# Kernel tuning notes

Measured on AMD Instinct MI355X. Metric: run time of the kernel, lower is better.

## Reference

```python
import jax, jax.numpy as jnp
import numpy as np

NUM_FREQS = 6

def posenc(x, num_freqs):
    freqs = (2.0 ** jnp.arange(num_freqs)).astype(x.dtype)  # [F]
    ang = x[..., None] * freqs                               # [N, D, F]
    enc = jnp.concatenate([jnp.sin(ang), jnp.cos(ang)], axis=-1)  # [N, D, 2F]
    return enc.reshape(x.shape[0], -1)

def setup_inputs() -> dict:
    key = jax.random.key(0)
    k1, k2, k3 = jax.random.split(key, 3)
    N, D, C = 200000, 6, 256
    E = D * 2 * NUM_FREQS  # 72
    X = jax.random.normal(k1, (N, D), dtype=jnp.float32)
    linear_mappings = jax.random.normal(k2, (3 * C, E), dtype=jnp.float32) * 0.05
    centroids = jax.random.normal(k3, (C, 3), dtype=jnp.float32)
    return {"X": X, "linear_mappings": linear_mappings, "centroids": centroids}

def reference(X, linear_mappings, centroids):
    N = X.shape[0]
    encoded_X = posenc(X, NUM_FREQS)                         # [N, E]
    rgb_clusters = encoded_X @ linear_mappings.T             # [N, 3C]
    rgb_clusters = rgb_clusters.reshape(N, -1, 3)            # [N, C, 3]
    # scores = centroids @ X[:, :3].T  -> softmax over clusters per point
    scores = X[:, :3] @ centroids.T                          # [N, C] (== scores.T in torch code)
    attention_weights = jax.nn.softmax(scores, axis=-1)      # [N, C]
    # torch does diagonal(attn @ rgb_clusters).T == per-row contraction:
    rgb = jnp.einsum('nc,ncd->nd', attention_weights, rgb_clusters)  # [N, 3]
    return rgb
```

## Files before the change

### kernel.cpp

```cpp
#include <hip/hip_runtime.h>
#include <math.h>


#define NCLUST   256
#define M_BLK    32
#define THREADS  64
#define NTILES   15
#define BG_BYTES (NTILES * 8 * 64 * 16)
#define ET_STRIDE 72

typedef __attribute__((ext_vector_type(8))) short bfrag_t;
typedef __attribute__((ext_vector_type(4))) float cfrag_t;
typedef __attribute__((ext_vector_type(4))) unsigned int uifrag_t;

static __device__ __forceinline__ unsigned short f2bf1(float f) {
    return __builtin_bit_cast(unsigned short, (__bf16)f);
}
static __device__ __forceinline__ unsigned int f2bf2(float lo, float hi) {
    return (unsigned int)f2bf1(lo) | ((unsigned int)f2bf1(hi) << 16);
}
static __device__ __forceinline__ float bf2f(unsigned short s) {
    return __uint_as_float(((unsigned int)s) << 16);
}

__global__ void prep_kernel(const float* __restrict__ W, uint4* __restrict__ Bg) {
    const int u = blockIdx.x * 256 + threadIdx.x;
    if (u >= NTILES * 8 * 64) return;
    const int lane = u & 63, ks = (u >> 6) & 7, tile = u >> 9;
    const int ln = lane & 15, q = lane >> 4;
    const int jp = tile * 16 + ln;
    const int d  = jp / 80;
    const int e  = jp - d * 80;
    const int c0 = ks * 32 + q * 8;
    unsigned int w[4] = {0u, 0u, 0u, 0u};
    if (e < 72) {
#pragma unroll
        for (int i = 0; i < 4; ++i) {
            float f0 = W[((c0 + 2 * i)     * 3 + d) * 72 + e];
            float f1 = W[((c0 + 2 * i + 1) * 3 + d) * 72 + e];
            w[i] = f2bf2(f0, f1);
        }
    }
    Bg[u] = make_uint4(w[0], w[1], w[2], w[3]);
}

#define MFMA2(KS, B) \
    a0 = __builtin_amdgcn_mfma_f32_16x16x32_bf16( \
             __builtin_bit_cast(bfrag_t, afrag[0][KS]), (B), a0, 0, 0, 0); \
    a1 = __builtin_amdgcn_mfma_f32_16x16x32_bf16( \
             __builtin_bit_cast(bfrag_t, afrag[1][KS]), (B), a1, 0, 0, 0);

__global__ __launch_bounds__(THREADS, 2) void rgb_attn_mfma(
    const float* __restrict__ X,
    const float* __restrict__ cent,
    const void* __restrict__ Bg,
    float* __restrict__ out, int N)
{
    __shared__ __align__(16) float Xs[M_BLK * 6];
    __shared__ __align__(16) unsigned char encT[80 * ET_STRIDE];

    const int lane = threadIdx.x;
    const int q    = lane >> 4;
    const int ln   = lane & 15;
    const int mbase = blockIdx.x * M_BLK;

    if (mbase + M_BLK <= N) {
        if (lane < 48) {
            const float4 v = *(const float4*)(X + (size_t)mbase * 6 + lane * 4);
            *(float4*)(Xs + lane * 4) = v;
        }
    } else {
#pragma unroll 1
        for (int i = lane; i < M_BLK * 6; i += 64) {
            const int p  = mbase + i / 6;
            const int pc = (p < N) ? p : (N - 1);
            Xs[i] = X[pc * 6 + (i % 6)];
        }
    }

    const char* Bgc = (const char*)Bg + lane * 16;
    bfrag_t b0 = *(const bfrag_t*)(Bgc + 0 * 1024);
    bfrag_t b1 = *(const bfrag_t*)(Bgc + 1 * 1024);
    bfrag_t b2 = *(const bfrag_t*)(Bgc + 2 * 1024);
    bfrag_t b3 = *(const bfrag_t*)(Bgc + 3 * 1024);
    bfrag_t b4 = *(const bfrag_t*)(Bgc + 4 * 1024);
    bfrag_t b5 = *(const bfrag_t*)(Bgc + 5 * 1024);
    bfrag_t b6 = *(const bfrag_t*)(Bgc + 6 * 1024);
    bfrag_t b7 = *(const bfrag_t*)(Bgc + 7 * 1024);

    {
        const int pt = lane & 31;
        const int h  = lane >> 5;
        unsigned char* colp = encT + pt * 2;
#pragma unroll
        for (int k = 0; k < 3; ++k) {
            const int dd = 3 * h + k;
            const float xv = Xs[pt * 6 + dd];
            float s[6], c[6];
            __sincosf(xv, &s[0], &c[0]);
#pragma unroll
            for (int f = 1; f < 6; ++f) {
                s[f] = 2.0f * s[f-1] * c[f-1];
                c[f] = 1.0f - 2.0f * s[f-1] * s[f-1];
            }
#pragma unroll
            for (int f = 0; f < 6; ++f) {
                *(unsigned short*)(colp + (dd*12 + f)     * ET_STRIDE) = f2bf1(s[f]);
                *(unsigned short*)(colp + (dd*12 + 6 + f) * ET_STRIDE) = f2bf1(c[f]);
            }
        }
        *(uint2*)(encT + (72 + (lane >> 3)) * ET_STRIDE + (lane & 7) * 8) = make_uint2(0u, 0u);
    }

    uifrag_t afrag[2][8];
    float dA = 0.0f, dB = 0.0f;
    {
        const float x00 = Xs[ln * 6 + 0], x01 = Xs[ln * 6 + 1], x02 = Xs[ln * 6 + 2];
        const float x10 = Xs[(16 + ln) * 6 + 0], x11 = Xs[(16 + ln) * 6 + 1],
                    x12 = Xs[(16 + ln) * 6 + 2];
        const float4* c4base = (const float4*)cent;
#pragma unroll
        for (int g = 0; g < 8; ++g) {
            const float4* c4 = c4base + (6 * q + 24 * g);
            const float4 v0 = c4[0], v1 = c4[1], v2 = c4[2];
            const float4 v3 = c4[3], v4 = c4[4], v5 = c4[5];
            float cx[8], cy[8], cz[8];
            cx[0]=v0.x; cy[0]=v0.y; cz[0]=v0.z;
            cx[1]=v0.w; cy[1]=v1.x; cz[1]=v1.y;
            cx[2]=v1.z; cy[2]=v1.w; cz[2]=v2.x;
            cx[3]=v2.y; cy[3]=v2.z; cz[3]=v2.w;
            cx[4]=v3.x; cy[4]=v3.y; cz[4]=v3.z;
            cx[5]=v3.w; cy[5]=v4.x; cz[5]=v4.y;
            cx[6]=v4.z; cy[6]=v4.w; cz[6]=v5.x;
            cx[7]=v5.y; cy[7]=v5.z; cz[7]=v5.w;
            float ea[8], eb[8];
#pragma unroll
            for (int j = 0; j < 8; ++j) {
                ea[j] = __expf(fmaf(x00, cx[j], fmaf(x01, cy[j], x02 * cz[j])));
                eb[j] = __expf(fmaf(x10, cx[j], fmaf(x11, cy[j], x12 * cz[j])));
                dA += ea[j]; dB += eb[j];
            }
#pragma unroll
            for (int w = 0; w < 4; ++w) {
                afrag[0][g][w] = f2bf2(ea[2*w], ea[2*w+1]);
                afrag[1][g][w] = f2bf2(eb[2*w], eb[2*w+1]);
            }
        }
    }

#pragma unroll
    for (int d = 0; d < 3; ++d) {
        float part2[2][4] = {};
#pragma unroll 1
        for (int tt = 0; tt < 5; ++tt) {
            const int t = d * 5 + tt;
            const char* bp = Bgc + (t + 1) * 8192;
            cfrag_t a0 = {0.f,0.f,0.f,0.f}, a1 = {0.f,0.f,0.f,0.f};

            MFMA2(0, b0) MFMA2(1, b1) MFMA2(2, b2) MFMA2(3, b3)
            if (t < NTILES - 1) {
                b0 = *(const bfrag_t*)(bp + 0 * 1024);
                b1 = *(const bfrag_t*)(bp + 1 * 1024);
                b2 = *(const bfrag_t*)(bp + 2 * 1024);
                b3 = *(const bfrag_t*)(bp + 3 * 1024);
            }

            MFMA2(4, b4) MFMA2(5, b5) MFMA2(6, b6) MFMA2(7, b7)
            if (t < NTILES - 1) {
                b4 = *(const bfrag_t*)(bp + 4 * 1024);
                b5 = *(const bfrag_t*)(bp + 5 * 1024);
                b6 = *(const bfrag_t*)(bp + 6 * 1024);
                b7 = *(const bfrag_t*)(bp + 7 * 1024);
            }

            const unsigned char* ep = encT + (tt * 16 + ln) * ET_STRIDE + q * 8;
#pragma unroll
            for (int mt = 0; mt < 2; ++mt) {
                const ushort4 ev = *(const ushort4*)(ep + mt * 32);
                const cfrag_t a = mt ? a1 : a0;
                part2[mt][0] = fmaf(a[0], bf2f(ev.x), part2[mt][0]);
                part2[mt][1] = fmaf(a[1], bf2f(ev.y), part2[mt][1]);
                part2[mt][2] = fmaf(a[2], bf2f(ev.z), part2[mt][2]);
                part2[mt][3] = fmaf(a[3], bf2f(ev.w), part2[mt][3]);
            }
        }

#pragma unroll
        for (int mask = 1; mask <= 8; mask <<= 1)
#pragma unroll
            for (int mt = 0; mt < 2; ++mt)
#pragma unroll
                for (int r = 0; r < 4; ++r)
                    part2[mt][r] += __shfl_xor(part2[mt][r], mask, 64);

        float sA = dA + __shfl_xor(dA, 16, 64); sA += __shfl_xor(sA, 32, 64);
        float sB = dB + __shfl_xor(dB, 16, 64); sB += __shfl_xor(sB, 32, 64);
        const float iA = 1.0f / sA;
        const float iB = 1.0f / sB;
        float invr[2][4];
#pragma unroll
        for (int r = 0; r < 4; ++r) {
            invr[0][r] = __shfl(iA, q * 4 + r, 64);
            invr[1][r] = __shfl(iB, q * 4 + r, 64);
        }

        if (ln == 0) {
#pragma unroll
            for (int mt = 0; mt < 2; ++mt)
#pragma unroll
                for (int r = 0; r < 4; ++r) {
                    const int pm = mt * 16 + q * 4 + r;
                    const int g  = mbase + pm;
                    if (g < N)
                        out[g * 3 + d] = part2[mt][r] * invr[mt][r];
                }
        }
    }
}

__global__ __launch_bounds__(256) void rgb_attn_fallback(
    const float* __restrict__ X, const float* __restrict__ W,
    const float* __restrict__ cent, float* __restrict__ out, int N)
{
    const int n = blockIdx.x * 256 + threadIdx.x;
    const bool valid = (n < N);
    float x[6];
#pragma unroll
    for (int k = 0; k < 6; ++k) x[k] = valid ? X[n * 6 + k] : 0.0f;
    float enc[72];
#pragma unroll
    for (int d = 0; d < 6; ++d)
#pragma unroll
        for (int f = 0; f < 6; ++f) {
            float s, c;
            __sincosf(x[d] * (float)(1 << f), &s, &c);
            enc[d*12+f] = s; enc[d*12+6+f] = c;
        }
    float acc0 = 0, acc1 = 0, acc2 = 0, denom = 0;
#pragma unroll 1
    for (int c = 0; c < NCLUST; ++c) {
        float s = fmaf(x[0], cent[c*3], fmaf(x[1], cent[c*3+1], x[2]*cent[c*3+2]));
        float ew = __expf(s);
        const float* w = W + c * 216;
        float d0 = 0, d1 = 0, d2 = 0;
#pragma unroll
        for (int e = 0; e < 72; ++e) {
            float ee = enc[e];
            d0 = fmaf(ee, w[e], d0);
            d1 = fmaf(ee, w[72 + e], d1);
            d2 = fmaf(ee, w[144 + e], d2);
        }
        denom += ew;
        acc0 = fmaf(ew, d0, acc0); acc1 = fmaf(ew, d1, acc1); acc2 = fmaf(ew, d2, acc2);
    }
    if (valid) {
        float inv = 1.0f / denom;
        out[n*3+0] = acc0*inv; out[n*3+1] = acc1*inv; out[n*3+2] = acc2*inv;
    }
}

extern "C" void kernel_launch(void* const* d_in, const int* in_sizes, int n_in,
                              void* d_out, int out_size, void* d_ws, size_t ws_size,
                              hipStream_t stream)
{
    const float* X    = (const float*)d_in[0];
    const float* W    = (const float*)d_in[1];
    const float* cent = (const float*)d_in[2];
    float* out = (float*)d_out;
    const int N = in_sizes[0] / 6;

    if (ws_size >= (size_t)BG_BYTES) {
        uint4* Bg = (uint4*)d_ws;
        prep_kernel<<<(NTILES * 8 * 64 + 255) / 256, 256, 0, stream>>>(W, Bg);
        const int blocks = (N + M_BLK - 1) / M_BLK;
        rgb_attn_mfma<<<blocks, THREADS, 0, stream>>>(X, cent, (const void*)Bg, out, N);
    } else {
        rgb_attn_fallback<<<(N + 255) / 256, 256, 0, stream>>>(X, W, cent, out, N);
    }
}
```

Baseline: 106.1 us.

## Share weight tiles across four waves via LDS staging with direct global-to-LDS loads

Each block now runs four wavefronts covering 128 points instead of one wave covering 32. The bf16 weight fragments for one output channel (five tiles) are staged into LDS with global_load_lds, and all waves share them instead of each wave streaming the weights from global or L2 into registers. This adds block-level barriers between the three channel phases and roughly 40KB of LDS per block. Occupancy may drop, and the reload between phases is not overlapped with compute.

```diff
diff --git a/kernel.cpp b/kernel.cpp
--- a/kernel.cpp
+++ b/kernel.cpp
@@ -3,8 +3,9 @@
 
 
 #define NCLUST   256
-#define M_BLK    32
-#define THREADS  64
+#define M_BLK    128
+#define WPTS     32
+#define THREADS  256
 #define NTILES   15
 #define BG_BYTES (NTILES * 8 * 64 * 16)
 #define ET_STRIDE 72
@@ -21,6 +22,11 @@
 }
 static __device__ __forceinline__ float bf2f(unsigned short s) {
     return __uint_as_float(((unsigned int)s) << 16);
+}
+static __device__ __forceinline__ void glds16(const void* g, void* l) {
+    __builtin_amdgcn_global_load_lds(
+        (const __attribute__((address_space(1))) unsigned int*)g,
+        (__attribute__((address_space(3))) unsigned int*)l, 16, 0, 0);
 }
 
 __global__ void prep_kernel(const float* __restrict__ W, uint4* __restrict__ Bg) {
@@ -50,43 +56,44 @@
     a1 = __builtin_amdgcn_mfma_f32_16x16x32_bf16( \
              __builtin_bit_cast(bfrag_t, afrag[1][KS]), (B), a1, 0, 0, 0);
 
-__global__ __launch_bounds__(THREADS, 2) void rgb_attn_mfma(
+__global__ __launch_bounds__(THREADS, 4) void rgb_attn_mfma(
     const float* __restrict__ X,
     const float* __restrict__ cent,
     const void* __restrict__ Bg,
     float* __restrict__ out, int N)
 {
-    __shared__ __align__(16) float Xs[M_BLK * 6];
-    __shared__ __align__(16) unsigned char encT[80 * ET_STRIDE];
-
-    const int lane = threadIdx.x;
+    __shared__ __align__(16) unsigned char Bt[5 * 8192];
+    __shared__ __align__(16) unsigned char encT4[4 * 80 * ET_STRIDE];
+    __shared__ __align__(16) float Xs4[4 * WPTS * 6];
+
+    const int tid  = threadIdx.x;
+    const int lane = tid & 63;
+    const int wv   = tid >> 6;
     const int q    = lane >> 4;
     const int ln   = lane & 15;
-    const int mbase = blockIdx.x * M_BLK;
-
-    if (mbase + M_BLK <= N) {
+    const int mbase = blockIdx.x * M_BLK + wv * WPTS;
+    float* Xs = Xs4 + wv * (WPTS * 6);
+    unsigned char* encT = encT4 + wv * (80 * ET_STRIDE);
+
+#pragma unroll
+    for (int i = 0; i < 10; ++i) {
+        const int u = i * 256 + tid;
+        glds16((const char*)Bg + u * 16, (char*)Bt + u * 16);
+    }
+
+    if (mbase + WPTS <= N) {
         if (lane < 48) {
             const float4 v = *(const float4*)(X + (size_t)mbase * 6 + lane * 4);
             *(float4*)(Xs + lane * 4) = v;
         }
     } else {
 #pragma unroll 1
-        for (int i = lane; i < M_BLK * 6; i += 64) {
+        for (int i = lane; i < WPTS * 6; i += 64) {
             const int p  = mbase + i / 6;
             const int pc = (p < N) ? p : (N - 1);
             Xs[i] = X[pc * 6 + (i % 6)];
         }
     }
-
-    const char* Bgc = (const char*)Bg + lane * 16;
-    bfrag_t b0 = *(const bfrag_t*)(Bgc + 0 * 1024);
-    bfrag_t b1 = *(const bfrag_t*)(Bgc + 1 * 1024);
-    bfrag_t b2 = *(const bfrag_t*)(Bgc + 2 * 1024);
-    bfrag_t b3 = *(const bfrag_t*)(Bgc + 3 * 1024);
-    bfrag_t b4 = *(const bfrag_t*)(Bgc + 4 * 1024);
-    bfrag_t b5 = *(const bfrag_t*)(Bgc + 5 * 1024);
-    bfrag_t b6 = *(const bfrag_t*)(Bgc + 6 * 1024);
-    bfrag_t b7 = *(const bfrag_t*)(Bgc + 7 * 1024);
 
     {
         const int pt = lane & 31;
@@ -148,30 +155,36 @@
         }
     }
 
+    __syncthreads();
+
 #pragma unroll
     for (int d = 0; d < 3; ++d) {
+        if (d) {
+            __syncthreads();
+#pragma unroll
+            for (int i = 0; i < 10; ++i) {
+                const int u = i * 256 + tid;
+                glds16((const char*)Bg + d * 40960 + u * 16, (char*)Bt + u * 16);
+            }
+            __syncthreads();
+        }
+
         float part2[2][4] = {};
 #pragma unroll 1
         for (int tt = 0; tt < 5; ++tt) {
-            const int t = d * 5 + tt;
-            const char* bp = Bgc + (t + 1) * 8192;
+            const unsigned char* bb = Bt + tt * 8192 + lane * 16;
             cfrag_t a0 = {0.f,0.f,0.f,0.f}, a1 = {0.f,0.f,0.f,0.f};
 
+            bfrag_t b0 = *(const bfrag_t*)(bb + 0 * 1024);
+            bfrag_t b1 = *(const bfrag_t*)(bb + 1 * 1024);
+            bfrag_t b2 = *(const bfrag_t*)(bb + 2 * 1024);
+            bfrag_t b3 = *(const bfrag_t*)(bb + 3 * 1024);
             MFMA2(0, b0) MFMA2(1, b1) MFMA2(2, b2) MFMA2(3, b3)
-            if (t < NTILES - 1) {
-                b0 = *(const bfrag_t*)(bp + 0 * 1024);
-                b1 = *(const bfrag_t*)(bp + 1 * 1024);
-                b2 = *(const bfrag_t*)(bp + 2 * 1024);
-                b3 = *(const bfrag_t*)(bp + 3 * 1024);
-            }
-
-            MFMA2(4, b4) MFMA2(5, b5) MFMA2(6, b6) MFMA2(7, b7)
-            if (t < NTILES - 1) {
-                b4 = *(const bfrag_t*)(bp + 4 * 1024);
-                b5 = *(const bfrag_t*)(bp + 5 * 1024);
-                b6 = *(const bfrag_t*)(bp + 6 * 1024);
-                b7 = *(const bfrag_t*)(bp + 7 * 1024);
-            }
+            b0 = *(const bfrag_t*)(bb + 4 * 1024);
+            b1 = *(const bfrag_t*)(bb + 5 * 1024);
+            b2 = *(const bfrag_t*)(bb + 6 * 1024);
+            b3 = *(const bfrag_t*)(bb + 7 * 1024);
+            MFMA2(4, b0) MFMA2(5, b1) MFMA2(6, b2) MFMA2(7, b3)
 
             const unsigned char* ep = encT + (tt * 16 + ln) * ET_STRIDE + q * 8;
 #pragma unroll
```

Result: no change. 107.5 us (+1.4%).
